# Optimization experiments

Measured on AMD Instinct MI355X. Metric: run time of the kernel, lower is better.

## Reference

```python
import jax, jax.numpy as jnp
import numpy as np

POOL_SIZES = (1, 3, 6, 8)
EPS = 1e-5


def conv1x1(x, W, b):
    # x: [b, cin, h, w], W: [cout, cin], b: [cout]
    return jnp.einsum('bchw,oc->bohw', x, W) + b[None, :, None, None]


def ppm(x):
    # x: [b, c, h, w] -> [b, c, S] with S = sum(p*p); H,W divisible by each p
    b, c, h, w = x.shape
    outs = []
    for p in POOL_SIZES:
        pooled = x.reshape(b, c, p, h // p, p, w // p).mean(axis=(3, 5))
        outs.append(pooled.reshape(b, c, p * p))
    return jnp.concatenate(outs, axis=-1)


def setup_inputs() -> dict:
    key = jax.random.key(0)
    ks = jax.random.split(key, 8)
    B, Cin, H, W = 4, 512, 120, 120
    Ck, Cv, Cout = 256, 256, 512
    x = jax.random.normal(ks[0], (B, Cin, H, W), dtype=jnp.float32)
    sc = lambda cin: 1.0 / np.sqrt(cin)
    Wk = jax.random.normal(ks[1], (Ck, Cin), dtype=jnp.float32) * sc(Cin)
    bk = jnp.zeros((Ck,), jnp.float32)
    gamma = jnp.ones((Ck,), jnp.float32)
    beta = jnp.zeros((Ck,), jnp.float32)
    mean = jax.random.normal(ks[2], (Ck,), dtype=jnp.float32) * 0.1
    var = jax.random.uniform(ks[3], (Ck,), dtype=jnp.float32, minval=0.5, maxval=1.5)
    Wv = jax.random.normal(ks[4], (Cv, Cin), dtype=jnp.float32) * sc(Cin)
    bv = jnp.zeros((Cv,), jnp.float32)
    # original inits Conv_Out to zero; use random weights for a nontrivial baseline
    Wo = jax.random.normal(ks[5], (Cout, Cv), dtype=jnp.float32) * sc(Cv)
    bo = jnp.zeros((Cout,), jnp.float32)
    return {'x': x, 'Wk': Wk, 'bk': bk, 'gamma': gamma, 'beta': beta,
            'mean': mean, 'var': var, 'Wv': Wv, 'bv': bv, 'Wo': Wo, 'bo': bo}


def reference(x, Wk, bk, gamma, beta, mean, var, Wv, bv, Wo, bo):
    b, _, h, w = x.shape
    ck = Wk.shape[0]
    cv = Wv.shape[0]
    # shared Conv_Key / Conv_Query: conv1x1 -> BN (inference) -> ReLU
    kq = conv1x1(x, Wk, bk)
    inv = gamma / jnp.sqrt(var + EPS)
    kq = jax.nn.relu(kq * inv[None, :, None, None] + (beta - mean * inv)[None, :, None, None])
    value = ppm(conv1x1(x, Wv, bv)).transpose(0, 2, 1)      # [b, S, cv]
    key = ppm(kq)                                            # [b, ck, S]
    query = kq.reshape(b, ck, h * w).transpose(0, 2, 1)      # [b, hw, ck]
    scores = jnp.einsum('bnc,bcs->bns', query, key) * (ck ** -0.5)
    attn = jax.nn.softmax(scores, axis=-1)                   # [b, hw, S]
    agg = jnp.einsum('bns,bsv->bnv', attn, value)            # [b, hw, cv]
    agg = agg.transpose(0, 2, 1).reshape(b, cv, h, w)
    return conv1x1(agg, Wo, bo)
```

## Files before the change

kernel.cpp:

```cpp
#include <hip/hip_runtime.h>
#include <cstdint>
#include <cstddef>

#define HW 14400
#define WIDTH 120
#define S_TOT 110

typedef unsigned short u16;
typedef __attribute__((ext_vector_type(8))) short bf16x8;
typedef __attribute__((ext_vector_type(4))) float f32x4;

__device__ __forceinline__ u16 f2bf(float x) {
  unsigned u = __float_as_uint(x);
  unsigned r = (u + 0x7fffu + ((u >> 16) & 1u)) >> 16;
  return (u16)r;
}
__device__ __forceinline__ float bf2f(u16 h) {
  return __uint_as_float((unsigned)h << 16);
}

__device__ __forceinline__ void async16(void* lds, const void* g) {
  __builtin_amdgcn_global_load_lds(
      (const __attribute__((address_space(1))) void*)g,
      (__attribute__((address_space(3))) void*)lds, 16, 0, 0);
}

__device__ __forceinline__ float pool_scale(int s) {
  return (s == 0) ? (1.f / 14400.f)
         : (s < 10) ? (1.f / 1600.f)
         : (s < 46) ? (1.f / 400.f)
                    : (1.f / 225.f);
}

__global__ __launch_bounds__(256) void pool_kernel(const float* __restrict__ in,
                                                   float* __restrict__ outp) {
  __shared__ float colsum[2880];
  __shared__ float part[576];
  const float* plane = in + (size_t)blockIdx.x * HW;
  int t = threadIdx.x;
  for (int i = t; i < 2880; i += 256) {
    int by = i / 120, x = i - by * 120;
    const float* p0 = plane + (by * 5) * WIDTH + x;
    colsum[i] = p0[0] + p0[WIDTH] + p0[2 * WIDTH] + p0[3 * WIDTH] + p0[4 * WIDTH];
  }
  __syncthreads();
  for (int bb = t; bb < 576; bb += 256) {
    int by = bb / 24, bx = bb - by * 24;
    const float* c = &colsum[by * 120 + bx * 5];
    part[bb] = c[0] + c[1] + c[2] + c[3] + c[4];
  }
  __syncthreads();
  if (t < S_TOT) {
    float s = 0.f;
    if (t == 0) {
      for (int i = 0; i < 576; ++i) s += part[i];
      s *= (1.f / 14400.f);
    } else if (t < 10) {
      int idx = t - 1, i = idx / 3, j = idx % 3;
      for (int a = 0; a < 8; ++a)
        for (int c = 0; c < 8; ++c) s += part[(i * 8 + a) * 24 + (j * 8 + c)];
      s *= (1.f / 1600.f);
    } else if (t < 46) {
      int idx = t - 10, i = idx / 6, j = idx % 6;
      for (int a = 0; a < 4; ++a)
        for (int c = 0; c < 4; ++c) s += part[(i * 4 + a) * 24 + (j * 4 + c)];
      s *= (1.f / 400.f);
    } else {
      int idx = t - 46, i = idx / 8, j = idx % 8;
      for (int a = 0; a < 3; ++a)
        for (int c = 0; c < 3; ++c) s += part[(i * 3 + a) * 24 + (j * 3 + c)];
      s *= (1.f / 225.f);
    }
    outp[(size_t)blockIdx.x * S_TOT + t] = s;
  }
}

__global__ __launch_bounds__(256) void convert_w(const float* __restrict__ in,
                                                 u16* __restrict__ hi,
                                                 u16* __restrict__ lo, int n) {
  int i = blockIdx.x * 256 + threadIdx.x;
  if (i < n) {
    float v = in[i];
    u16 h = f2bf(v);
    hi[i] = h;
    lo[i] = f2bf(v - bf2f(h));
  }
}

template <int CIN>
__global__ __launch_bounds__(256) void convert_t(const float* __restrict__ X,
                                                 u16* __restrict__ xth,
                                                 u16* __restrict__ xtl) {
  __shared__ float ls[64][65];
  int b = blockIdx.z;
  int n0 = blockIdx.x * 64, k0 = blockIdx.y * 64;
  int t = threadIdx.x;
  int rt = t >> 4, c4 = (t & 15) * 4;
#pragma unroll
  for (int rr = 0; rr < 4; ++rr) {
    int kk = rr * 16 + rt;
    float4 v = *(const float4*)&X[((size_t)(b * CIN + k0 + kk)) * HW + n0 + c4];
    ls[kk][c4] = v.x; ls[kk][c4 + 1] = v.y; ls[kk][c4 + 2] = v.z; ls[kk][c4 + 3] = v.w;
  }
  __syncthreads();
#pragma unroll
  for (int rr = 0; rr < 4; ++rr) {
    int nn = rr * 16 + rt;
    float v0 = ls[c4 + 0][nn], v1 = ls[c4 + 1][nn], v2 = ls[c4 + 2][nn], v3 = ls[c4 + 3][nn];
    ushort4 oh, ol;
    oh.x = f2bf(v0); ol.x = f2bf(v0 - bf2f(oh.x));
    oh.y = f2bf(v1); ol.y = f2bf(v1 - bf2f(oh.y));
    oh.z = f2bf(v2); ol.z = f2bf(v2 - bf2f(oh.z));
    oh.w = f2bf(v3); ol.w = f2bf(v3 - bf2f(oh.w));
    size_t idx = ((size_t)(b * HW + n0 + nn)) * CIN + k0 + c4;
    *(ushort4*)&xth[idx] = oh;
    *(ushort4*)&xtl[idx] = ol;
  }
}

template <int K, int M_TOT, bool BNRELU>
__global__ __launch_bounds__(512, 2) void gemm_mfma(
    const u16* __restrict__ Ah, const u16* __restrict__ Al,
    const u16* __restrict__ Bh, const u16* __restrict__ Bl,
    float* __restrict__ C,
    const float* __restrict__ p0, const float* __restrict__ p1,
    const float* __restrict__ p2, const float* __restrict__ p3,
    const float* __restrict__ p4,
    u16* __restrict__ Th, u16* __restrict__ Tl) {
  constexpr int NSTEP = K / 32;
  __shared__ alignas(16) u16 smem[61440];

  int t = threadIdx.x, w = t >> 6, l = t & 63;
  int wm = w >> 2, wn = w & 3;
  int b = blockIdx.z;
  int n0 = blockIdx.x * 192;
  int m0 = blockIdx.y * 128;

  int fr = l & 15, fkc = l >> 4;
  const size_t bOff = (size_t)b * HW;

  auto stage = [&](int ks, int slot) {
    int k0 = ks * 32;
#pragma unroll
    for (int c = 0; c < 5; ++c) {
      int i = w * 5 + c;
      const u16* g;
      u16* d;
      if (i < 8) {
        g = Ah + (size_t)(m0 + i * 16 + fr) * K + k0 + fkc * 8;
        d = &smem[slot * 8192 + i * 512];
      } else if (i < 16) {
        g = Al + (size_t)(m0 + (i - 8) * 16 + fr) * K + k0 + fkc * 8;
        d = &smem[slot * 8192 + i * 512];
      } else if (i < 28) {
        g = Bh + (bOff + n0 + (i - 16) * 16 + fr) * (size_t)K + k0 + fkc * 8;
        d = &smem[24576 + slot * 12288 + (i - 16) * 512];
      } else {
        g = Bl + (bOff + n0 + (i - 28) * 16 + fr) * (size_t)K + k0 + fkc * 8;
        d = &smem[24576 + slot * 12288 + (i - 16) * 512];
      }
      async16(d, g);
    }
  };

  f32x4 acc[4][3];
#pragma unroll
  for (int i = 0; i < 4; ++i)
#pragma unroll
    for (int j = 0; j < 3; ++j) acc[i][j] = (f32x4){0.f, 0.f, 0.f, 0.f};

  stage(0, 0);
  stage(1, 1);

  for (int ks = 0; ks < NSTEP; ++ks) {
    if (ks + 1 < NSTEP)
      asm volatile("s_waitcnt vmcnt(5)" ::: "memory");
    else
      asm volatile("s_waitcnt vmcnt(0)" ::: "memory");
    __builtin_amdgcn_s_barrier();
    __builtin_amdgcn_sched_barrier(0);

    if (ks + 2 < NSTEP) stage(ks + 2, (ks + 2) % 3);

    int cur = ks % 3;
    bf16x8 bh[3], bl[3];
#pragma unroll
    for (int nt = 0; nt < 3; ++nt) {
      bh[nt] = *(const bf16x8*)&smem[24576 + cur * 12288 + (wn * 3 + nt) * 512 + l * 8];
      bl[nt] = *(const bf16x8*)&smem[24576 + cur * 12288 + (12 + wn * 3 + nt) * 512 + l * 8];
    }
    bf16x8 ah[4], al[4];
#pragma unroll
    for (int mt = 0; mt < 4; ++mt) {
      ah[mt] = *(const bf16x8*)&smem[cur * 8192 + (wm * 4 + mt) * 512 + l * 8];
      al[mt] = *(const bf16x8*)&smem[cur * 8192 + (8 + wm * 4 + mt) * 512 + l * 8];
    }
    __builtin_amdgcn_s_setprio(1);
#pragma unroll
    for (int mt = 0; mt < 4; ++mt)
#pragma unroll
      for (int nt = 0; nt < 3; ++nt) {
        acc[mt][nt] = __builtin_amdgcn_mfma_f32_16x16x32_bf16(ah[mt], bh[nt], acc[mt][nt], 0, 0, 0);
        acc[mt][nt] = __builtin_amdgcn_mfma_f32_16x16x32_bf16(ah[mt], bl[nt], acc[mt][nt], 0, 0, 0);
        acc[mt][nt] = __builtin_amdgcn_mfma_f32_16x16x32_bf16(al[mt], bh[nt], acc[mt][nt], 0, 0, 0);
      }
    __builtin_amdgcn_s_setprio(0);
  }

  __syncthreads();

  int q4 = (l >> 4) * 4;
#pragma unroll
  for (int mt = 0; mt < 4; ++mt) {
    int mb = m0 + (wm * 4 + mt) * 16 + q4;
    float iv[4], ad[4];
    if (BNRELU) {
      float4 g0 = *(const float4*)&p0[mb];
      float4 g1 = *(const float4*)&p1[mb];
      float4 g2 = *(const float4*)&p2[mb];
      float4 g3 = *(const float4*)&p3[mb];
      float4 g4 = *(const float4*)&p4[mb];
      iv[0] = g1.x * rsqrtf(g4.x + 1e-5f);
      iv[1] = g1.y * rsqrtf(g4.y + 1e-5f);
      iv[2] = g1.z * rsqrtf(g4.z + 1e-5f);
      iv[3] = g1.w * rsqrtf(g4.w + 1e-5f);
      ad[0] = (g0.x - g3.x) * iv[0] + g2.x;
      ad[1] = (g0.y - g3.y) * iv[1] + g2.y;
      ad[2] = (g0.z - g3.z) * iv[2] + g2.z;
      ad[3] = (g0.w - g3.w) * iv[3] + g2.w;
    } else {
      float4 g0 = *(const float4*)&p0[mb];
      ad[0] = g0.x; ad[1] = g0.y; ad[2] = g0.z; ad[3] = g0.w;
    }
#pragma unroll
    for (int nt = 0; nt < 3; ++nt) {
      int n = n0 + (wn * 3 + nt) * 16 + fr;
      float v[4];
#pragma unroll
      for (int r = 0; r < 4; ++r) {
        float x = acc[mt][nt][r];
        v[r] = BNRELU ? fmaxf(x * iv[r] + ad[r], 0.f) : x + ad[r];
        if (C) C[((size_t)(b * M_TOT) + mb + r) * HW + n] = v[r];
      }
      if (BNRELU && Th) {
        ushort4 hh, ll;
        hh.x = f2bf(v[0]); ll.x = f2bf(v[0] - bf2f(hh.x));
        hh.y = f2bf(v[1]); ll.y = f2bf(v[1] - bf2f(hh.y));
        hh.z = f2bf(v[2]); ll.z = f2bf(v[2] - bf2f(hh.z));
        hh.w = f2bf(v[3]); ll.w = f2bf(v[3] - bf2f(hh.w));
        int nl = (wn * 3 + nt) * 16 + fr;
        int ml = (wm * 4 + mt) * 16 + q4;
        *(ushort4*)&smem[nl * 136 + ml] = hh;
        *(ushort4*)&smem[26112 + nl * 136 + ml] = ll;
      }
    }
  }
  if (BNRELU && Th) {
    __syncthreads();
#pragma unroll
    for (int it = 0; it < 6; ++it) {
      int row = it * 32 + (t >> 4);
      int c8 = (t & 15) * 8;
      size_t go = (bOff + n0 + row) * (size_t)M_TOT + m0 + c8;
      *(bf16x8*)&Th[go] = *(const bf16x8*)&smem[row * 136 + c8];
      *(bf16x8*)&Tl[go] = *(const bf16x8*)&smem[26112 + row * 136 + c8];
    }
  }
}

__global__ __launch_bounds__(256) void pool_kqt(const u16* __restrict__ kqth,
                                                const u16* __restrict__ kqtl,
                                                float* __restrict__ keypsum) {
  int cq = blockIdx.x, band = blockIdx.y, b = blockIdx.z;
  int t = threadIdx.x;
  int row0 = band * 5, col0 = cq * 30;
  int r3 = row0 / 40, r6 = row0 / 20, r8 = row0 / 15;
  float* base = keypsum + (size_t)b * 110 * 256 + t;
  float s1 = 0.f, s3 = 0.f, s6 = 0.f, s8 = 0.f;
  int b3 = -1, b6 = -1, b8 = -1;
  for (int cc = 0; cc < 30; ++cc) {
    int col = col0 + cc;
    float v = 0.f;
#pragma unroll
    for (int r = 0; r < 5; ++r) {
      size_t o = ((size_t)(b * HW + (row0 + r) * 120 + col)) * 256 + t;
      v += bf2f(kqth[o]) + bf2f(kqtl[o]);
    }
    int i3 = 1 + r3 * 3 + col / 40;
    int i6 = 10 + r6 * 6 + col / 20;
    int i8 = 46 + r8 * 8 + col / 15;
    s1 += v;
    if (i3 != b3) { if (b3 >= 0) atomicAdd(base + (size_t)b3 * 256, s3); s3 = 0.f; b3 = i3; }
    s3 += v;
    if (i6 != b6) { if (b6 >= 0) atomicAdd(base + (size_t)b6 * 256, s6); s6 = 0.f; b6 = i6; }
    s6 += v;
    if (i8 != b8) { if (b8 >= 0) atomicAdd(base + (size_t)b8 * 256, s8); s8 = 0.f; b8 = i8; }
    s8 += v;
  }
  atomicAdd(base, s1);
  atomicAdd(base + (size_t)b3 * 256, s3);
  atomicAdd(base + (size_t)b6 * 256, s6);
  atomicAdd(base + (size_t)b8 * 256, s8);
}

__global__ __launch_bounds__(256) void value_kernel(
    const float* __restrict__ Wv, const float* __restrict__ xp,
    const float* __restrict__ bv, u16* __restrict__ vth,
    u16* __restrict__ vtl) {
  int b = blockIdx.x >> 7, s = blockIdx.x & 127;
  int t = threadIdx.x;
  size_t o = ((size_t)(b * 256 + t)) * 128 + s;
  if (s >= S_TOT) { vth[o] = 0; vtl[o] = 0; return; }
  __shared__ float xs[512];
  for (int i = t; i < 512; i += 256) xs[i] = xp[((size_t)b * 512 + i) * S_TOT + s];
  __syncthreads();
  float accv = 0.f;
  const float* wv = Wv + (size_t)t * 512;
  for (int k = 0; k < 512; k += 4) {
    float4 w4 = *(const float4*)&wv[k];
    accv += w4.x * xs[k] + w4.y * xs[k + 1] + w4.z * xs[k + 2] + w4.w * xs[k + 3];
  }
  accv += bv[t];
  u16 h = f2bf(accv);
  vth[o] = h;
  vtl[o] = f2bf(accv - bf2f(h));
}

template <int SUMLAYOUT>
__global__ __launch_bounds__(256) void convert_key(const float* __restrict__ keyp,
                                                   u16* __restrict__ kth,
                                                   u16* __restrict__ ktl) {
  int b = blockIdx.x;
  int t = threadIdx.x;
  for (int i = t; i < 128 * 256; i += 256) {
    int s = i >> 8, c = i & 255;
    float v = 0.f;
    if (s < S_TOT) {
      if (SUMLAYOUT)
        v = keyp[((size_t)(b * 110 + s)) * 256 + c] * pool_scale(s);
      else
        v = keyp[((size_t)(b * 256 + c)) * S_TOT + s];
    }
    u16 h = f2bf(v);
    size_t o = ((size_t)(b * 128 + s)) * 256 + c;
    kth[o] = h;
    ktl[o] = f2bf(v - bf2f(h));
  }
}

__global__ __launch_bounds__(256) void attn_mfma(
    const u16* __restrict__ qh, const u16* __restrict__ ql,
    const u16* __restrict__ kh, const u16* __restrict__ kl,
    const u16* __restrict__ vh, const u16* __restrict__ vl,
    u16* __restrict__ aggh, u16* __restrict__ aggl) {
  __shared__ alignas(16) u16 lds[17408];
  int b = blockIdx.y, pix0 = blockIdx.x * 64;
  int t = threadIdx.x, w = t >> 6, l = t & 63;
  int fr = l & 15, q = l >> 4;

  const u16* kbase_h = kh + (size_t)b * 128 * 256;
  const u16* kbase_l = kl + (size_t)b * 128 * 256;

  f32x4 acc[8];
#pragma unroll
  for (int st = 0; st < 8; ++st) acc[st] = (f32x4){0.f, 0.f, 0.f, 0.f};

  const u16* qbh = qh + ((size_t)(b * HW + pix0 + w * 16 + fr)) * 256 + q * 8;
  const u16* qbl = ql + ((size_t)(b * HW + pix0 + w * 16 + fr)) * 256 + q * 8;

  auto stageK = [&](int ks, int buf) {
    int c0 = ks * 32;
#pragma unroll
    for (int j = 0; j < 4; ++j) {
      int i = t + j * 256;
      int half = i >> 9;
      int idx = i & 511;
      int st = idx >> 6, ll = idx & 63;
      const u16* src = (half ? kbase_l : kbase_h) +
                       (st * 16 + (ll & 15)) * 256 + c0 + (ll >> 4) * 8;
      async16(&lds[buf * 8192 + half * 4096 + idx * 8], src);
    }
  };

  stageK(0, 0);
  for (int ks = 0; ks < 8; ++ks) {
    __syncthreads();
    if (ks < 7) stageK(ks + 1, (ks + 1) & 1);
    bf16x8 ah = *(const bf16x8*)(qbh + ks * 32);
    bf16x8 al = *(const bf16x8*)(qbl + ks * 32);
    const u16* kb = &lds[(ks & 1) * 8192 + l * 8];
#pragma unroll
    for (int st = 0; st < 8; ++st) {
      bf16x8 bh = *(const bf16x8*)(kb + st * 512);
      bf16x8 bl = *(const bf16x8*)(kb + 4096 + st * 512);
      acc[st] = __builtin_amdgcn_mfma_f32_16x16x32_bf16(ah, bh, acc[st], 0, 0, 0);
      acc[st] = __builtin_amdgcn_mfma_f32_16x16x32_bf16(ah, bl, acc[st], 0, 0, 0);
      acc[st] = __builtin_amdgcn_mfma_f32_16x16x32_bf16(al, bh, acc[st], 0, 0, 0);
    }
  }

#pragma unroll
  for (int st = 0; st < 8; ++st)
#pragma unroll
    for (int r = 0; r < 4; ++r) acc[st][r] *= 0.0625f;
  if (fr >= 14) {
#pragma unroll
    for (int r = 0; r < 4; ++r) acc[6][r] = -1e30f;
  }
#pragma unroll
  for (int r = 0; r < 4; ++r) acc[7][r] = -1e30f;

#pragma unroll
  for (int r = 0; r < 4; ++r) {
    float m = -1e30f;
#pragma unroll
    for (int st = 0; st < 8; ++st) m = fmaxf(m, acc[st][r]);
    m = fmaxf(m, __shfl_xor(m, 1));
    m = fmaxf(m, __shfl_xor(m, 2));
    m = fmaxf(m, __shfl_xor(m, 4));
    m = fmaxf(m, __shfl_xor(m, 8));
    float s = 0.f;
#pragma unroll
    for (int st = 0; st < 8; ++st) {
      float e = __expf(acc[st][r] - m);
      acc[st][r] = e;
      s += e;
    }
    s += __shfl_xor(s, 1);
    s += __shfl_xor(s, 2);
    s += __shfl_xor(s, 4);
    s += __shfl_xor(s, 8);
    float inv = 1.f / s;
#pragma unroll
    for (int st = 0; st < 8; ++st) acc[st][r] *= inv;
  }

  __syncthreads();

  int prow = w * 16 + q * 4;
#pragma unroll
  for (int st = 0; st < 8; ++st) {
    int s = st * 16 + fr;
#pragma unroll
    for (int r = 0; r < 4; ++r) {
      float v = acc[st][r];
      u16 h = f2bf(v);
      lds[(prow + r) * 136 + s] = h;
      lds[8704 + (prow + r) * 136 + s] = f2bf(v - bf2f(h));
    }
  }
  __syncthreads();

  f32x4 oacc[4][4];
#pragma unroll
  for (int nt = 0; nt < 4; ++nt)
#pragma unroll
    for (int pt = 0; pt < 4; ++pt) oacc[nt][pt] = (f32x4){0.f, 0.f, 0.f, 0.f};

  const u16* vbh = vh + ((size_t)(b * 256 + w * 64 + fr)) * 128 + q * 8;
  const u16* vbl = vl + ((size_t)(b * 256 + w * 64 + fr)) * 128 + q * 8;

#pragma unroll
  for (int kc = 0; kc < 4; ++kc) {
    bf16x8 ph[4], pl[4];
#pragma unroll
    for (int pt = 0; pt < 4; ++pt) {
      ph[pt] = *(const bf16x8*)&lds[(pt * 16 + fr) * 136 + kc * 32 + q * 8];
      pl[pt] = *(const bf16x8*)&lds[8704 + (pt * 16 + fr) * 136 + kc * 32 + q * 8];
    }
#pragma unroll
    for (int nt = 0; nt < 4; ++nt) {
      bf16x8 a_h = *(const bf16x8*)(vbh + (size_t)nt * 16 * 128 + kc * 32);
      bf16x8 a_l = *(const bf16x8*)(vbl + (size_t)nt * 16 * 128 + kc * 32);
#pragma unroll
      for (int pt = 0; pt < 4; ++pt) {
        oacc[nt][pt] = __builtin_amdgcn_mfma_f32_16x16x32_bf16(a_h, ph[pt], oacc[nt][pt], 0, 0, 0);
        oacc[nt][pt] = __builtin_amdgcn_mfma_f32_16x16x32_bf16(a_h, pl[pt], oacc[nt][pt], 0, 0, 0);
        oacc[nt][pt] = __builtin_amdgcn_mfma_f32_16x16x32_bf16(a_l, ph[pt], oacc[nt][pt], 0, 0, 0);
      }
    }
  }

#pragma unroll
  for (int nt = 0; nt < 4; ++nt) {
#pragma unroll
    for (int pt = 0; pt < 4; ++pt) {
      ushort4 oh, ol;
      float v0 = oacc[nt][pt][0], v1 = oacc[nt][pt][1];
      float v2 = oacc[nt][pt][2], v3 = oacc[nt][pt][3];
      oh.x = f2bf(v0); ol.x = f2bf(v0 - bf2f(oh.x));
      oh.y = f2bf(v1); ol.y = f2bf(v1 - bf2f(oh.y));
      oh.z = f2bf(v2); ol.z = f2bf(v2 - bf2f(oh.z));
      oh.w = f2bf(v3); ol.w = f2bf(v3 - bf2f(oh.w));
      size_t o = ((size_t)(b * HW + pix0 + pt * 16 + fr)) * 256 + (w * 4 + nt) * 16 + q * 4;
      *(ushort4*)&aggh[o] = oh;
      *(ushort4*)&aggl[o] = ol;
    }
  }
}

extern "C" void kernel_launch(void* const* d_in, const int* in_sizes, int n_in,
                              void* d_out, int out_size, void* d_ws, size_t ws_size,
                              hipStream_t stream) {
  (void)in_sizes; (void)n_in; (void)out_size;
  const float* x     = (const float*)d_in[0];
  const float* Wk    = (const float*)d_in[1];
  const float* bk    = (const float*)d_in[2];
  const float* gamma = (const float*)d_in[3];
  const float* beta  = (const float*)d_in[4];
  const float* mean  = (const float*)d_in[5];
  const float* var   = (const float*)d_in[6];
  const float* Wv    = (const float*)d_in[7];
  const float* bv    = (const float*)d_in[8];
  const float* Wo    = (const float*)d_in[9];
  const float* bo    = (const float*)d_in[10];
  float* out = (float*)d_out;

  char* p = (char*)d_ws;
  float* kq = (float*)p;      p += (size_t)14745600 * 4;
  u16* xth = (u16*)p;         p += (size_t)29491200 * 2;
  u16* xtl = (u16*)p;         p += (size_t)29491200 * 2;
  u16* wkh = (u16*)p;         p += 131072 * 2;
  u16* wkl = (u16*)p;         p += 131072 * 2;
  u16* woh = (u16*)p;         p += 131072 * 2;
  u16* wol = (u16*)p;         p += 131072 * 2;
  float* xp = (float*)p;      p += (size_t)4 * 512 * 110 * 4;
  float* keypsum = (float*)p; p += (size_t)4 * 110 * 256 * 4;
  u16* vth = (u16*)p;         p += (size_t)4 * 256 * 128 * 2;
  u16* vtl = (u16*)p;         p += (size_t)4 * 256 * 128 * 2;
  u16* kth = (u16*)p;         p += (size_t)4 * 128 * 256 * 2;
  u16* ktl = (u16*)p;         p += (size_t)4 * 128 * 256 * 2;
  u16* kqth_f = (u16*)p;      p += (size_t)14745600 * 2;
  u16* kqtl_f = (u16*)p;      p += (size_t)14745600 * 2;
  bool fused = ((size_t)(p - (char*)d_ws) <= ws_size);

  u16* aggh = xth;
  u16* aggl = xtl;
  u16* kqth = fused ? kqth_f : xth + (size_t)14745600;
  u16* kqtl = fused ? kqtl_f : xtl + (size_t)14745600;

  if (fused)
    hipMemsetAsync(keypsum, 0, (size_t)4 * 110 * 256 * 4, stream);

  convert_w<<<512, 256, 0, stream>>>(Wk, wkh, wkl, 256 * 512);
  convert_w<<<512, 256, 0, stream>>>(Wo, woh, wol, 512 * 256);
  convert_t<512><<<dim3(225, 8, 4), 256, 0, stream>>>(x, xth, xtl);
  pool_kernel<<<dim3(4 * 512), dim3(256), 0, stream>>>(x, xp);
  value_kernel<<<dim3(4 * 128), 256, 0, stream>>>(Wv, xp, bv, vth, vtl);
  gemm_mfma<512, 256, true><<<dim3(75, 2, 4), 512, 0, stream>>>(
      wkh, wkl, xth, xtl, fused ? nullptr : kq, bk, gamma, beta, mean, var,
      fused ? kqth : (u16*)nullptr, fused ? kqtl : (u16*)nullptr);
  if (fused) {
    pool_kqt<<<dim3(4, 24, 4), 256, 0, stream>>>(kqth, kqtl, keypsum);
    convert_key<1><<<dim3(4), dim3(256), 0, stream>>>(keypsum, kth, ktl);
  } else {
    convert_t<256><<<dim3(225, 4, 4), 256, 0, stream>>>(kq, kqth, kqtl);
    pool_kernel<<<dim3(4 * 256), dim3(256), 0, stream>>>(kq, keypsum);
    convert_key<0><<<dim3(4), dim3(256), 0, stream>>>(keypsum, kth, ktl);
  }
  attn_mfma<<<dim3(225, 4), 256, 0, stream>>>(kqth, kqtl, kth, ktl, vth, vtl,
                                              aggh, aggl);
  gemm_mfma<256, 512, false><<<dim3(75, 4, 4), 512, 0, stream>>>(
      woh, wol, aggh, aggl, out, bo, nullptr, nullptr, nullptr, nullptr,
      nullptr, nullptr);
}
```

Measured before the change: 566.3 us.

## Fuse fp32-to-bf16 split of x into the key GEMM's B-tile loading

Adds a key-projection GEMM that reads fp32 x directly from global memory into registers, splits each value into hi/lo bf16 and writes the pieces to LDS inside the software pipeline. This removes the separate convert_t pass over x on the fused path. The convert_t pass wrote transposed hi/lo copies and the GEMM then read them back. The cost is strided scalar fp32 loads and conversion ALU work inside the GEMM main loop, which may hurt its pipelining. One catch: aggh/aggl alias xth/xtl, so that buffer is still used later as scratch.

```diff
diff --git a/kernel.cpp b/kernel.cpp
--- a/kernel.cpp
+++ b/kernel.cpp
@@ -268,6 +268,184 @@
   }
 }
 
+__global__ __launch_bounds__(512) void gemm_kq_fx(
+    const u16* __restrict__ Ah, const u16* __restrict__ Al,
+    const float* __restrict__ X,
+    float* __restrict__ C,
+    const float* __restrict__ p0, const float* __restrict__ p1,
+    const float* __restrict__ p2, const float* __restrict__ p3,
+    const float* __restrict__ p4,
+    u16* __restrict__ Th, u16* __restrict__ Tl) {
+  constexpr int NSTEP = 16;
+  __shared__ alignas(16) u16 smem[52224];
+
+  int t = threadIdx.x, w = t >> 6, l = t & 63;
+  int wm = w >> 2, wn = w & 3;
+  int b = blockIdx.z;
+  int n0 = blockIdx.x * 192;
+  int m0 = blockIdx.y * 128;
+  int fr = l & 15, fkc = l >> 4;
+  const size_t bOff = (size_t)b * HW;
+  const float* xb = X + (size_t)b * 512 * HW + n0;
+
+  int kc4v[3], nnv[3], wOffH[3];
+#pragma unroll
+  for (int j = 0; j < 3; ++j) {
+    int s = t + j * 512;
+    kc4v[j] = s / 192;
+    nnv[j] = s - kc4v[j] * 192;
+    wOffH[j] = (nnv[j] >> 4) * 512 + (((kc4v[j] >> 1) * 16 + (nnv[j] & 15)) * 8) +
+               (kc4v[j] & 1) * 4;
+  }
+
+  auto stageA = [&](int ks, int slot) {
+    int k0 = ks * 32;
+#pragma unroll
+    for (int c = 0; c < 2; ++c) {
+      int i = w * 2 + c;
+      const u16* g = (i < 8)
+          ? Ah + (size_t)(m0 + i * 16 + fr) * 512 + k0 + fkc * 8
+          : Al + (size_t)(m0 + (i - 8) * 16 + fr) * 512 + k0 + fkc * 8;
+      async16(&smem[slot * 8192 + i * 512], g);
+    }
+  };
+
+  auto issueB = [&](int ks, float* r) {
+#pragma unroll
+    for (int j = 0; j < 3; ++j) {
+      const float* src = xb + (size_t)(ks * 32 + kc4v[j] * 4) * HW + nnv[j];
+#pragma unroll
+      for (int i = 0; i < 4; ++i) r[j * 4 + i] = src[(size_t)i * HW];
+    }
+  };
+
+  auto cvtB = [&](float* r, int buf) {
+#pragma unroll
+    for (int j = 0; j < 3; ++j) {
+      ushort4 hh, ll;
+      float v0 = r[j * 4 + 0], v1 = r[j * 4 + 1], v2 = r[j * 4 + 2], v3 = r[j * 4 + 3];
+      hh.x = f2bf(v0); ll.x = f2bf(v0 - bf2f(hh.x));
+      hh.y = f2bf(v1); ll.y = f2bf(v1 - bf2f(hh.y));
+      hh.z = f2bf(v2); ll.z = f2bf(v2 - bf2f(hh.z));
+      hh.w = f2bf(v3); ll.w = f2bf(v3 - bf2f(hh.w));
+      int o = 24576 + buf * 12288 + wOffH[j];
+      *(ushort4*)&smem[o] = hh;
+      *(ushort4*)&smem[o + 12 * 512] = ll;
+    }
+  };
+
+  f32x4 acc[4][3];
+#pragma unroll
+  for (int i = 0; i < 4; ++i)
+#pragma unroll
+    for (int j = 0; j < 3; ++j) acc[i][j] = (f32x4){0.f, 0.f, 0.f, 0.f};
+
+  float rB0[12], rB1[12];
+  stageA(0, 0); issueB(0, rB0);
+  stageA(1, 1); issueB(1, rB1);
+  __builtin_amdgcn_sched_barrier(0);
+  asm volatile("s_waitcnt vmcnt(14)" ::: "memory");
+  cvtB(rB0, 0);
+
+#pragma unroll 2
+  for (int ks = 0; ks < NSTEP; ++ks) {
+    asm volatile("s_waitcnt lgkmcnt(0)" ::: "memory");
+    __builtin_amdgcn_s_barrier();
+    __builtin_amdgcn_sched_barrier(0);
+
+    if (ks + 2 < NSTEP) {
+      stageA(ks + 2, (ks + 2) % 3);
+      issueB(ks + 2, (ks & 1) ? rB1 : rB0);
+      __builtin_amdgcn_sched_barrier(0);
+    }
+
+    int curA = ks % 3, curB = ks & 1;
+    bf16x8 bh[3], bl[3];
+#pragma unroll
+    for (int nt = 0; nt < 3; ++nt) {
+      bh[nt] = *(const bf16x8*)&smem[24576 + curB * 12288 + (wn * 3 + nt) * 512 + l * 8];
+      bl[nt] = *(const bf16x8*)&smem[24576 + curB * 12288 + (12 + wn * 3 + nt) * 512 + l * 8];
+    }
+    bf16x8 ah[4], al[4];
+#pragma unroll
+    for (int mt = 0; mt < 4; ++mt) {
+      ah[mt] = *(const bf16x8*)&smem[curA * 8192 + (wm * 4 + mt) * 512 + l * 8];
+      al[mt] = *(const bf16x8*)&smem[curA * 8192 + (8 + wm * 4 + mt) * 512 + l * 8];
+    }
+    __builtin_amdgcn_s_setprio(1);
+#pragma unroll
+    for (int mt = 0; mt < 4; ++mt)
+#pragma unroll
+      for (int nt = 0; nt < 3; ++nt) {
+        acc[mt][nt] = __builtin_amdgcn_mfma_f32_16x16x32_bf16(ah[mt], bh[nt], acc[mt][nt], 0, 0, 0);
+        acc[mt][nt] = __builtin_amdgcn_mfma_f32_16x16x32_bf16(ah[mt], bl[nt], acc[mt][nt], 0, 0, 0);
+        acc[mt][nt] = __builtin_amdgcn_mfma_f32_16x16x32_bf16(al[mt], bh[nt], acc[mt][nt], 0, 0, 0);
+      }
+    __builtin_amdgcn_s_setprio(0);
+
+    if (ks + 1 < NSTEP) {
+      if (ks + 2 < NSTEP)
+        asm volatile("s_waitcnt vmcnt(14)" ::: "memory");
+      else
+        asm volatile("s_waitcnt vmcnt(0)" ::: "memory");
+      cvtB((ks & 1) ? rB0 : rB1, (ks + 1) & 1);
+    }
+  }
+
+  __syncthreads();
+
+  int q4 = (l >> 4) * 4;
+#pragma unroll
+  for (int mt = 0; mt < 4; ++mt) {
+    int mb = m0 + (wm * 4 + mt) * 16 + q4;
+    float iv[4], ad[4];
+    {
+      float4 g0 = *(const float4*)&p0[mb];
+      float4 g1 = *(const float4*)&p1[mb];
+      float4 g2 = *(const float4*)&p2[mb];
+      float4 g3 = *(const float4*)&p3[mb];
+      float4 g4 = *(const float4*)&p4[mb];
+      iv[0] = g1.x * rsqrtf(g4.x + 1e-5f);
+      iv[1] = g1.y * rsqrtf(g4.y + 1e-5f);
+      iv[2] = g1.z * rsqrtf(g4.z + 1e-5f);
+      iv[3] = g1.w * rsqrtf(g4.w + 1e-5f);
+      ad[0] = (g0.x - g3.x) * iv[0] + g2.x;
+      ad[1] = (g0.y - g3.y) * iv[1] + g2.y;
+      ad[2] = (g0.z - g3.z) * iv[2] + g2.z;
+      ad[3] = (g0.w - g3.w) * iv[3] + g2.w;
+    }
+#pragma unroll
+    for (int nt = 0; nt < 3; ++nt) {
+      int n = n0 + (wn * 3 + nt) * 16 + fr;
+      float v[4];
+#pragma unroll
+      for (int r = 0; r < 4; ++r) {
+        float x = acc[mt][nt][r];
+        v[r] = fmaxf(x * iv[r] + ad[r], 0.f);
+        if (C) C[((size_t)(b * 256) + mb + r) * HW + n] = v[r];
+      }
+      ushort4 hh, ll;
+      hh.x = f2bf(v[0]); ll.x = f2bf(v[0] - bf2f(hh.x));
+      hh.y = f2bf(v[1]); ll.y = f2bf(v[1] - bf2f(hh.y));
+      hh.z = f2bf(v[2]); ll.z = f2bf(v[2] - bf2f(hh.z));
+      hh.w = f2bf(v[3]); ll.w = f2bf(v[3] - bf2f(hh.w));
+      int nl = (wn * 3 + nt) * 16 + fr;
+      int ml = (wm * 4 + mt) * 16 + q4;
+      *(ushort4*)&smem[nl * 136 + ml] = hh;
+      *(ushort4*)&smem[26112 + nl * 136 + ml] = ll;
+    }
+  }
+  __syncthreads();
+#pragma unroll
+  for (int it = 0; it < 6; ++it) {
+    int row = it * 32 + (t >> 4);
+    int c8 = (t & 15) * 8;
+    size_t go = (bOff + n0 + row) * (size_t)256 + m0 + c8;
+    *(bf16x8*)&Th[go] = *(const bf16x8*)&smem[row * 136 + c8];
+    *(bf16x8*)&Tl[go] = *(const bf16x8*)&smem[26112 + row * 136 + c8];
+  }
+}
+
 __global__ __launch_bounds__(256) void pool_kqt(const u16* __restrict__ kqth,
                                                 const u16* __restrict__ kqtl,
                                                 float* __restrict__ keypsum) {
@@ -544,16 +722,17 @@
 
   convert_w<<<512, 256, 0, stream>>>(Wk, wkh, wkl, 256 * 512);
   convert_w<<<512, 256, 0, stream>>>(Wo, woh, wol, 512 * 256);
-  convert_t<512><<<dim3(225, 8, 4), 256, 0, stream>>>(x, xth, xtl);
   pool_kernel<<<dim3(4 * 512), dim3(256), 0, stream>>>(x, xp);
   value_kernel<<<dim3(4 * 128), 256, 0, stream>>>(Wv, xp, bv, vth, vtl);
-  gemm_mfma<512, 256, true><<<dim3(75, 2, 4), 512, 0, stream>>>(
-      wkh, wkl, xth, xtl, fused ? nullptr : kq, bk, gamma, beta, mean, var,
-      fused ? kqth : (u16*)nullptr, fused ? kqtl : (u16*)nullptr);
   if (fused) {
+    gemm_kq_fx<<<dim3(75, 2, 4), 512, 0, stream>>>(
+        wkh, wkl, x, nullptr, bk, gamma, beta, mean, var, kqth, kqtl);
     pool_kqt<<<dim3(4, 24, 4), 256, 0, stream>>>(kqth, kqtl, keypsum);
     convert_key<1><<<dim3(4), dim3(256), 0, stream>>>(keypsum, kth, ktl);
   } else {
+    convert_t<512><<<dim3(225, 8, 4), 256, 0, stream>>>(x, xth, xtl);
+    gemm_mfma<512, 256, true><<<dim3(75, 2, 4), 512, 0, stream>>>(
+        wkh, wkl, xth, xtl, kq, bk, gamma, beta, mean, var, kqth, kqtl);
     convert_t<256><<<dim3(225, 4, 4), 256, 0, stream>>>(kq, kqth, kqtl);
     pool_kernel<<<dim3(4 * 256), dim3(256), 0, stream>>>(kq, keypsum);
     convert_key<0><<<dim3(4), dim3(256), 0, stream>>>(keypsum, kth, ktl);
```

New measurement: 524.2 us. 1.08x faster.
